# Kernel optimization log

Hardware: AMD Instinct MI355X
Metric: run time of the kernel (lower is better)

## Reference

```python
import jax, jax.numpy as jnp
import numpy as np

KERNEL_MUL = 2.0
KERNEL_NUM = 5


def _cross_entropy(logits, labels):
    logp = jax.nn.log_softmax(logits, axis=-1)
    return -jnp.take_along_axis(logp, labels[:, None], axis=-1).mean()


def _distill_loss(teacher_logits, student_logits):
    t = jax.nn.softmax(teacher_logits, axis=-1)
    return jnp.sum(-t * jax.nn.log_softmax(student_logits, axis=-1), axis=-1).mean()


def _mk_mmd(source, target):
    # Multi-kernel Gaussian MMD (standard DAN-style implementation).
    ns = source.shape[0]
    total = jnp.concatenate([source, target], axis=0)  # [ns+nt, D]
    sq = jnp.sum(total * total, axis=1)
    l2 = sq[:, None] + sq[None, :] - 2.0 * (total @ total.T)  # [n, n]
    n = total.shape[0]
    bandwidth = jnp.sum(l2) / (n * n - n)
    bandwidth = bandwidth / (KERNEL_MUL ** (KERNEL_NUM // 2))
    kernels = jnp.zeros_like(l2)
    for i in range(KERNEL_NUM):
        kernels = kernels + jnp.exp(-l2 / (bandwidth * (KERNEL_MUL ** i)))
    xx = kernels[:ns, :ns]
    yy = kernels[ns:, ns:]
    xy = kernels[:ns, ns:]
    yx = kernels[ns:, :ns]
    return jnp.mean(xx + yy - xy - yx)


def setup_inputs() -> dict:
    key = jax.random.key(0)
    k1, k2, k3, k4, k5 = jax.random.split(key, 5)
    Ns, Nt, D, C = 4096, 4096, 256, 6
    return {
        "source_feature": jax.random.normal(k1, (Ns, D), dtype=jnp.float32),
        "target_feature": jax.random.normal(k2, (Nt, D), dtype=jnp.float32),
        "source_clf": jax.random.normal(k3, (Ns, C), dtype=jnp.float32),
        "target_clf": jax.random.normal(k4, (Nt, C), dtype=jnp.float32),
        "source_label": jax.random.randint(k5, (Ns,), 0, C, dtype=jnp.int64),
    }


def reference(source_feature, target_feature, source_clf, target_clf, source_label):
    clf_loss = _cross_entropy(source_clf, source_label)

    # Pairwise euclidean distance [Ns, Nt] (cdist, p=2)
    ss = jnp.sum(source_feature * source_feature, axis=1)
    tt = jnp.sum(target_feature * target_feature, axis=1)
    d2 = ss[:, None] + tt[None, :] - 2.0 * (source_feature @ target_feature.T)
    dist = jnp.sqrt(jnp.maximum(d2, 0.0))

    min_idx = jnp.argmin(dist, axis=1)    # nearest target for each source
    min_idx_t = jnp.argmin(dist, axis=0)  # nearest source for each target

    dis_loss = _distill_loss(source_clf, target_clf[min_idx, :])
    dis_loss = dis_loss + _distill_loss(source_clf[min_idx_t, :], target_clf)

    transfer_loss = _mk_mmd(source_feature, target_feature)
    return jnp.stack([clf_loss, dis_loss, transfer_loss])
```

## Files before the change

kernel.cpp:

```cpp
#include <hip/hip_runtime.h>
#include <hip/hip_bf16.h>


#define NS 4096
#define D  256
#define C  6

typedef unsigned int u32;
typedef unsigned short u16;
typedef __attribute__((ext_vector_type(8))) short short8;
typedef __attribute__((ext_vector_type(8))) unsigned short ushort8v;
typedef __attribute__((ext_vector_type(4))) float floatx4;
typedef __attribute__((ext_vector_type(2))) float float2v;

#define EXP2F(x) __builtin_amdgcn_exp2f(x)

#define GLD_LDS16(g, l)                                                        \
    __builtin_amdgcn_global_load_lds(                                          \
        (const __attribute__((address_space(1))) unsigned int*)(g),            \
        (__attribute__((address_space(3))) unsigned int*)(l), 16, 0, 0)

__device__ inline u16 f2bf(float f) {
    unsigned u = __float_as_uint(f);
    return (u16)((u + 0x7FFFu + ((u >> 16) & 1u)) >> 16);
}

__global__ __launch_bounds__(256) void kA(const float* __restrict__ src,
                                          const float* __restrict__ tgt,
                                          u16* __restrict__ sb, u16* __restrict__ tb,
                                          float* __restrict__ sq,
                                          u32* __restrict__ rowkey,
                                          u32* __restrict__ colkey,
                                          double* __restrict__ accD,
                                          int* __restrict__ cnts,
                                          float* __restrict__ ssqPart) {
    __shared__ float wsA[4];
    int b = blockIdx.x, t = threadIdx.x;
    int w = t >> 6, l = t & 63;
    int r2 = b * 4 + w;
    int r = r2 * 2 + (l >> 5);
    int lc = (l & 31) * 8;
    const float* row = (r < NS) ? src + (size_t)r * D : tgt + (size_t)(r - NS) * D;
    u16* orow        = (r < NS) ? sb + (size_t)r * D : tb + (size_t)(r - NS) * D;
    float4 v0 = *(const float4*)&row[lc];
    float4 v1 = *(const float4*)&row[lc + 4];
    ushort8v o;
    o.s0 = f2bf(v0.x); o.s1 = f2bf(v0.y); o.s2 = f2bf(v0.z); o.s3 = f2bf(v0.w);
    o.s4 = f2bf(v1.x); o.s5 = f2bf(v1.y); o.s6 = f2bf(v1.z); o.s7 = f2bf(v1.w);
    *(ushort8v*)&orow[lc] = o;
    float s = v0.x * v0.x + v0.y * v0.y + v0.z * v0.z + v0.w * v0.w +
              v1.x * v1.x + v1.y * v1.y + v1.z * v1.z + v1.w * v1.w;
    #pragma unroll
    for (int off = 16; off; off >>= 1) s += __shfl_down(s, off, 64);
    if ((l & 31) == 0) sq[r] = s;

    float rtot = s + __shfl_down(s, 32, 64);
    if (l == 0) wsA[w] = rtot;

    int gid = b * 256 + t;
    if (gid < NS) rowkey[gid] = 0xFFFFFFFFu;
    else if (gid < 2 * NS) colkey[gid - NS] = 0xFFFFFFFFu;
    if (b == 0) {
        if (t < 8) accD[t] = 0.0;
        else if (t == 8) cnts[0] = 0;
    }
    __syncthreads();
    if (t == 0) ssqPart[b] = wsA[0] + wsA[1] + wsA[2] + wsA[3];
}

__global__ __launch_bounds__(256, 3) void k3_mfma(const u16* __restrict__ Sb,
                                                  const u16* __restrict__ Tb,
                                                  const float* __restrict__ sq,
                                                  double* __restrict__ accD,
                                                  u32* __restrict__ rowkey,
                                                  u32* __restrict__ colkey,
                                                  const float* __restrict__ ssqPart) {
    int idx = blockIdx.x;
    int bz, ti, tj;
    if (idx < 1024) {
        bz = 0; ti = idx >> 5; tj = idx & 31;
    } else {
        int t = idx - 1024;
        bz = 1;
        if (t >= 528) { t -= 528; bz = 2; }
        int i = (int)((65.0f - sqrtf(4225.0f - 8.0f * (float)t)) * 0.5f);
        if ((i + 1) * (64 - i) / 2 <= t) i++;
        else if (i * (65 - i) / 2 > t) i--;
        ti = i;
        tj = i + (t - i * (65 - i) / 2);
    }

    const u16* Am = (bz == 2) ? Tb : Sb;
    const u16* Bm = (bz == 1) ? Sb : Tb;
    const float* sqA = (bz == 2) ? sq + NS : sq;
    const float* sqB = (bz == 1) ? sq : sq + NS;
    int zacc = (bz == 0) ? 2 : (bz - 1);

    __shared__ __align__(16) u16 Atile[128 * 64];
    __shared__ __align__(16) u16 Btile[128 * 64];
    __shared__ float sqa_s[128], sqb_s[128];
    __shared__ u32 rminL[128], cminL[128];
    __shared__ float wsum[4];
    __shared__ float wssq[4];

    int tid = threadIdx.x;
    int w = tid >> 6, ln = tid & 63;
    int wm = w >> 1, wn = w & 1;
    int quad = ln >> 4, lrow = ln & 15;
    int row0 = ti * 128, col0 = tj * 128;

    if (tid < 128) { sqa_s[tid] = sqA[row0 + tid]; rminL[tid] = 0xFFFFFFFFu; }
    else           { sqb_s[tid - 128] = sqB[col0 + tid - 128]; cminL[tid - 128] = 0xFFFFFFFFu; }

    float4 pv = *(const float4*)&ssqPart[tid * 4];
    float ssq_p = pv.x + pv.y + pv.z + pv.w;
    #pragma unroll
    for (int off = 32; off; off >>= 1) ssq_p += __shfl_down(ssq_p, off, 64);
    if (ln == 0) wssq[w] = ssq_p;

    int lr8 = ln >> 3;
    int cg  = (ln & 7) ^ lr8;

    floatx4 acc[4][4] = {};

    #pragma unroll 2
    for (int kc = 0; kc < D; kc += 64) {
        #pragma unroll
        for (int i = 0; i < 4; i++) {
            int lrb = w * 32 + i * 8;
            GLD_LDS16(Am + (size_t)(row0 + lrb + lr8) * D + kc + cg * 8,
                      &Atile[lrb * 64]);
            GLD_LDS16(Bm + (size_t)(col0 + lrb + lr8) * D + kc + cg * 8,
                      &Btile[lrb * 64]);
        }
        __syncthreads();
        #pragma unroll
        for (int ks = 0; ks < 2; ks++) {
            int ch = (ks * 4 + quad) ^ (lrow & 7);
            short8 bf4[4];
            #pragma unroll
            for (int cf = 0; cf < 4; cf++)
                bf4[cf] = *(const short8*)&Btile[(wn * 64 + cf * 16 + lrow) * 64 + ch * 8];
            #pragma unroll
            for (int rf = 0; rf < 4; rf++) {
                short8 af = *(const short8*)&Atile[(wm * 64 + rf * 16 + lrow) * 64 + ch * 8];
                #pragma unroll
                for (int cf = 0; cf < 4; cf++)
                    acc[rf][cf] = __builtin_amdgcn_mfma_f32_16x16x32_bf16(
                        af, bf4[cf], acc[rf][cf], 0, 0, 0);
            }
        }
        __syncthreads();
    }

    float ssq = wssq[0] + wssq[1] + wssq[2] + wssq[3];
    float bw = (float)(2.0 * 8192.0 * (double)ssq / (8192.0 * 8192.0 - 8192.0) / 4.0);
    float nlog = -1.4426950408889634f / (bw * 16.0f);
    float m2n  = -2.0f * nlog;
    float2v m2n2 = {m2n, m2n};
    float2v tsum2 = {0.f, 0.f};
    float tsum = 0.f;

    float sbn_c[4];
    #pragma unroll
    for (int cf = 0; cf < 4; cf++)
        sbn_c[cf] = sqb_s[wn * 64 + cf * 16 + lrow] * nlog;

    int rbase = row0 + wm * 64, cbase = col0 + wn * 64;

    if (bz == 0) {
        u32 ck[4];
        #pragma unroll
        for (int cf = 0; cf < 4; cf++) ck[cf] = 0xFFFFFFFFu;
        #pragma unroll
        for (int rf = 0; rf < 4; rf++) {
            int sA = wm * 64 + rf * 16 + quad * 4;
            int giB = rbase + rf * 16 + quad * 4;
            float2v san01 = {sqa_s[sA + 0] * nlog, sqa_s[sA + 1] * nlog};
            float2v san23 = {sqa_s[sA + 2] * nlog, sqa_s[sA + 3] * nlog};
            u32 rk[4];
            #pragma unroll
            for (int reg = 0; reg < 4; reg++) rk[reg] = 0xFFFFFFFFu;
            #pragma unroll
            for (int cf = 0; cf < 4; cf++) {
                int gj = cbase + cf * 16 + lrow;
                float2v sbv2 = {sbn_c[cf], sbn_c[cf]};
                float2v g01 = acc[rf][cf].xy * m2n2 + (san01 + sbv2);
                float2v g23 = acc[rf][cf].zw * m2n2 + (san23 + sbv2);
                float2v t4a, t4b;
                t4a.x = EXP2F(g01.x); t4a.y = EXP2F(g01.y);
                t4b.x = EXP2F(g23.x); t4b.y = EXP2F(g23.y);
                float2v t3a = t4a * t4a, t2a = t3a * t3a, t1a = t2a * t2a, t0a = t1a * t1a;
                float2v t3b = t4b * t4b, t2b = t3b * t3b, t1b = t2b * t2b, t0b = t1b * t1b;
                tsum2 += ((t0a + t1a) + (t2a + t3a)) + t4a;
                tsum2 += ((t0b + t1b) + (t2b + t3b)) + t4b;
                u32 q0 = __float_as_uint(g01.x) & 0xFFFFF000u;
                u32 q1 = __float_as_uint(g01.y) & 0xFFFFF000u;
                u32 q2 = __float_as_uint(g23.x) & 0xFFFFF000u;
                u32 q3 = __float_as_uint(g23.y) & 0xFFFFF000u;
                rk[0] = min(rk[0], q0 | (u32)gj);
                rk[1] = min(rk[1], q1 | (u32)gj);
                rk[2] = min(rk[2], q2 | (u32)gj);
                rk[3] = min(rk[3], q3 | (u32)gj);
                ck[cf] = min(ck[cf], q0 | (u32)(giB + 0));
                ck[cf] = min(ck[cf], q1 | (u32)(giB + 1));
                ck[cf] = min(ck[cf], q2 | (u32)(giB + 2));
                ck[cf] = min(ck[cf], q3 | (u32)(giB + 3));
            }
            #pragma unroll
            for (int reg = 0; reg < 4; reg++) {
                u32 v = rk[reg];
                #pragma unroll
                for (int m = 1; m <= 8; m <<= 1)
                    v = min(v, (u32)__shfl_xor((int)v, m, 64));
                if (lrow == 0)
                    atomicMin(&rminL[wm * 64 + rf * 16 + quad * 4 + reg], v);
            }
        }
        #pragma unroll
        for (int cf = 0; cf < 4; cf++) {
            u32 v = ck[cf];
            v = min(v, (u32)__shfl_xor((int)v, 16, 64));
            v = min(v, (u32)__shfl_xor((int)v, 32, 64));
            if (quad == 0)
                atomicMin(&cminL[wn * 64 + cf * 16 + lrow], v);
        }
    } else if (ti < tj) {
        #pragma unroll
        for (int rf = 0; rf < 4; rf++) {
            int sA = wm * 64 + rf * 16 + quad * 4;
            float2v san01 = {sqa_s[sA + 0] * nlog, sqa_s[sA + 1] * nlog};
            float2v san23 = {sqa_s[sA + 2] * nlog, sqa_s[sA + 3] * nlog};
            #pragma unroll
            for (int cf = 0; cf < 4; cf++) {
                float2v sbv2 = {sbn_c[cf], sbn_c[cf]};
                float2v g01 = acc[rf][cf].xy * m2n2 + (san01 + sbv2);
                float2v g23 = acc[rf][cf].zw * m2n2 + (san23 + sbv2);
                float2v t4a, t4b;
                t4a.x = EXP2F(g01.x); t4a.y = EXP2F(g01.y);
                t4b.x = EXP2F(g23.x); t4b.y = EXP2F(g23.y);
                float2v t3a = t4a * t4a, t2a = t3a * t3a, t1a = t2a * t2a, t0a = t1a * t1a;
                float2v t3b = t4b * t4b, t2b = t3b * t3b, t1b = t2b * t2b, t0b = t1b * t1b;
                tsum2 += ((t0a + t1a) + (t2a + t3a)) + t4a;
                tsum2 += ((t0b + t1b) + (t2b + t3b)) + t4b;
            }
        }
    } else {
        #pragma unroll
        for (int rf = 0; rf < 4; rf++) {
            float san[4];
            #pragma unroll
            for (int reg = 0; reg < 4; reg++)
                san[reg] = sqa_s[wm * 64 + rf * 16 + quad * 4 + reg] * nlog;
            #pragma unroll
            for (int cf = 0; cf < 4; cf++) {
                int gj = cbase + cf * 16 + lrow;
                float sbv = sbn_c[cf];
                #pragma unroll
                for (int reg = 0; reg < 4; reg++) {
                    int gi = rbase + rf * 16 + quad * 4 + reg;
                    float arg = fmaf(acc[rf][cf][reg], m2n, san[reg] + sbv);
                    float t4 = EXP2F(arg);
                    float t3 = t4 * t4, t2 = t3 * t3, t1 = t2 * t2, t0 = t1 * t1;
                    if (gi < gj)
                        tsum += t0 + t1 + t2 + t3 + t4;
                }
            }
        }
    }

    tsum += tsum2.x + tsum2.y;
    #pragma unroll
    for (int off = 32; off; off >>= 1) tsum += __shfl_down(tsum, off, 64);
    if (ln == 0) wsum[w] = tsum;
    __syncthreads();
    if (tid == 0)
        atomicAdd(&accD[zacc], (double)(wsum[0] + wsum[1] + wsum[2] + wsum[3]));
    if (bz == 0) {
        if (tid < 128) atomicMin(&rowkey[row0 + tid], rminL[tid]);
        else           atomicMin(&colkey[col0 + tid - 128], cminL[tid - 128]);
    }
}

__global__ __launch_bounds__(256) void k4(const float* __restrict__ sclf,
                                          const float* __restrict__ tclf,
                                          const int* __restrict__ label,
                                          const u32* __restrict__ rowkey,
                                          const u32* __restrict__ colkey,
                                          double* __restrict__ accD,
                                          int* __restrict__ cnts,
                                          float* __restrict__ out) {
    if (blockIdx.x == 16) {
        if (threadIdx.x == 0) {
            while (atomicAdd(&cnts[0], 0) < 16) __builtin_amdgcn_s_sleep(2);
            double Sxx  = atomicAdd(&accD[0], 0.0);
            double Syy  = atomicAdd(&accD[1], 0.0);
            double Sxy  = atomicAdd(&accD[2], 0.0);
            double clfS = atomicAdd(&accD[3], 0.0);
            double disS = atomicAdd(&accD[4], 0.0);
            double ns = (double)NS;
            out[0] = (float)(clfS / ns);
            out[1] = (float)(disS / ns);
            double sum_xx = 2.0 * Sxx + ns * 5.0;
            double sum_yy = 2.0 * Syy + ns * 5.0;
            out[2] = (float)((sum_xx + sum_yy - 2.0 * Sxy) / (ns * ns));
        }
        return;
    }

    int i = blockIdx.x * 256 + threadIdx.x;
    float clf, dis = 0.f;

    const float* x = sclf + (size_t)i * C;
    float mx = x[0];
    #pragma unroll
    for (int c = 1; c < C; c++) mx = fmaxf(mx, x[c]);
    float sx = 0.f;
    #pragma unroll
    for (int c = 0; c < C; c++) sx += __expf(x[c] - mx);
    clf = mx + __logf(sx) - x[label[i]];

    {
        int j = (int)(rowkey[i] & 0xFFFu);
        const float* y = tclf + (size_t)j * C;
        float my = y[0];
        #pragma unroll
        for (int c = 1; c < C; c++) my = fmaxf(my, y[c]);
        float sy = 0.f;
        #pragma unroll
        for (int c = 0; c < C; c++) sy += __expf(y[c] - my);
        float dot = 0.f;
        #pragma unroll
        for (int c = 0; c < C; c++) dot += __expf(x[c] - mx) * y[c];
        dis += my + __logf(sy) - dot / sx;
    }
    {
        int it = (int)(colkey[i] & 0xFFFu);
        const float* xt = sclf + (size_t)it * C;
        float mt = xt[0];
        #pragma unroll
        for (int c = 1; c < C; c++) mt = fmaxf(mt, xt[c]);
        float st = 0.f;
        #pragma unroll
        for (int c = 0; c < C; c++) st += __expf(xt[c] - mt);
        const float* zz = tclf + (size_t)i * C;
        float mz = zz[0];
        #pragma unroll
        for (int c = 1; c < C; c++) mz = fmaxf(mz, zz[c]);
        float sz = 0.f;
        #pragma unroll
        for (int c = 0; c < C; c++) sz += __expf(zz[c] - mz);
        float dot2 = 0.f;
        #pragma unroll
        for (int c = 0; c < C; c++) dot2 += __expf(xt[c] - mt) * zz[c];
        dis += mz + __logf(sz) - dot2 / st;
    }

    #pragma unroll
    for (int off = 32; off; off >>= 1) {
        clf += __shfl_down(clf, off, 64);
        dis += __shfl_down(dis, off, 64);
    }
    if ((threadIdx.x & 63) == 0) {
        atomicAdd(&accD[3], (double)clf);
        atomicAdd(&accD[4], (double)dis);
    }
    __syncthreads();
    if (threadIdx.x == 0) atomicAdd(&cnts[0], 1);
}

extern "C" void kernel_launch(void* const* d_in, const int* in_sizes, int n_in,
                              void* d_out, int out_size, void* d_ws, size_t ws_size,
                              hipStream_t stream) {
    const float* src  = (const float*)d_in[0];
    const float* tgt  = (const float*)d_in[1];
    const float* sclf = (const float*)d_in[2];
    const float* tclf = (const float*)d_in[3];
    const int*   lab  = (const int*)d_in[4];
    float* out = (float*)d_out;

    char* ws = (char*)d_ws;
    u16* sb     = (u16*)ws;
    u16* tb     = sb + (size_t)NS * D;
    u32* rowkey = (u32*)(ws + 2 * (size_t)NS * D * 2);
    u32* colkey = rowkey + NS;
    float* sq   = (float*)(colkey + NS);
    double* accD = (double*)((char*)sq + 2 * NS * 4 + 64);
    int* cnts    = (int*)(accD + 8);
    float* ssqPart = (float*)(accD + 16);

    kA<<<1024, 256, 0, stream>>>(src, tgt, sb, tb, sq, rowkey, colkey, accD, cnts, ssqPart);
    k3_mfma<<<2080, 256, 0, stream>>>(sb, tb, sq, accD, rowkey, colkey, ssqPart);
    k4<<<17, 256, 0, stream>>>(sclf, tclf, lab, rowkey, colkey, accD, cnts, out);
}
```

Baseline: 113.5 us.

## Fuse final loss kernel into MFMA kernel using completion counters

Removes the separate k4 launch by appending 17 extra blocks to the MFMA kernel grid. Sixteen of them spin on a counter until all 1024 cross-distance tiles have published their argmin keys, then compute the classification and distillation losses. The last block waits for all tiles and loss blocks before writing the outputs. This saves one launch and lets the loss work overlap with the MMD tiles, but it relies on in-kernel spin-waits, which could deadlock or waste CU slots if the waiting blocks get scheduled before the tiles they wait on.

```diff
diff --git a/kernel.cpp b/kernel.cpp
--- a/kernel.cpp
+++ b/kernel.cpp
@@ -62,7 +62,7 @@
     else if (gid < 2 * NS) colkey[gid - NS] = 0xFFFFFFFFu;
     if (b == 0) {
         if (t < 8) accD[t] = 0.0;
-        else if (t == 8) cnts[0] = 0;
+        else if (t >= 8 && t < 12) cnts[t - 8] = 0;
     }
     __syncthreads();
     if (t == 0) ssqPart[b] = wsA[0] + wsA[1] + wsA[2] + wsA[3];
@@ -74,8 +74,104 @@
                                                   double* __restrict__ accD,
                                                   u32* __restrict__ rowkey,
                                                   u32* __restrict__ colkey,
-                                                  const float* __restrict__ ssqPart) {
+                                                  const float* __restrict__ ssqPart,
+                                                  const float* __restrict__ sclf,
+                                                  const float* __restrict__ tclf,
+                                                  const int* __restrict__ label,
+                                                  int* __restrict__ cnts,
+                                                  float* __restrict__ out) {
     int idx = blockIdx.x;
+    int tid = threadIdx.x;
+
+    if (idx >= 2080) {
+        int widx = idx - 2080;
+        if (widx < 16) {
+            if (tid == 0)
+                while (atomicAdd(&cnts[0], 0) < 1024) __builtin_amdgcn_s_sleep(8);
+            __syncthreads();
+
+            int i = widx * 256 + tid;
+            float clf, dis = 0.f;
+
+            const float* x = sclf + (size_t)i * C;
+            float mx = x[0];
+            #pragma unroll
+            for (int c = 1; c < C; c++) mx = fmaxf(mx, x[c]);
+            float sx = 0.f;
+            #pragma unroll
+            for (int c = 0; c < C; c++) sx += __expf(x[c] - mx);
+            clf = mx + __logf(sx) - x[label[i]];
+
+            u32 rkv = atomicAdd(&rowkey[i], 0u);
+            u32 ckv = atomicAdd(&colkey[i], 0u);
+
+            {
+                int j = (int)(rkv & 0xFFFu);
+                const float* y = tclf + (size_t)j * C;
+                float my = y[0];
+                #pragma unroll
+                for (int c = 1; c < C; c++) my = fmaxf(my, y[c]);
+                float sy = 0.f;
+                #pragma unroll
+                for (int c = 0; c < C; c++) sy += __expf(y[c] - my);
+                float dot = 0.f;
+                #pragma unroll
+                for (int c = 0; c < C; c++) dot += __expf(x[c] - mx) * y[c];
+                dis += my + __logf(sy) - dot / sx;
+            }
+            {
+                int it = (int)(ckv & 0xFFFu);
+                const float* xt = sclf + (size_t)it * C;
+                float mt = xt[0];
+                #pragma unroll
+                for (int c = 1; c < C; c++) mt = fmaxf(mt, xt[c]);
+                float st = 0.f;
+                #pragma unroll
+                for (int c = 0; c < C; c++) st += __expf(xt[c] - mt);
+                const float* zz = tclf + (size_t)i * C;
+                float mz = zz[0];
+                #pragma unroll
+                for (int c = 1; c < C; c++) mz = fmaxf(mz, zz[c]);
+                float sz = 0.f;
+                #pragma unroll
+                for (int c = 0; c < C; c++) sz += __expf(zz[c] - mz);
+                float dot2 = 0.f;
+                #pragma unroll
+                for (int c = 0; c < C; c++) dot2 += __expf(xt[c] - mt) * zz[c];
+                dis += mz + __logf(sz) - dot2 / st;
+            }
+
+            #pragma unroll
+            for (int off = 32; off; off >>= 1) {
+                clf += __shfl_down(clf, off, 64);
+                dis += __shfl_down(dis, off, 64);
+            }
+            if ((tid & 63) == 0) {
+                atomicAdd(&accD[3], (double)clf);
+                atomicAdd(&accD[4], (double)dis);
+            }
+            __syncthreads();
+            if (tid == 0) atomicAdd(&cnts[2], 1);
+        } else {
+            if (tid == 0) {
+                while (atomicAdd(&cnts[1], 0) < 2080 ||
+                       atomicAdd(&cnts[2], 0) < 16) __builtin_amdgcn_s_sleep(8);
+                double Sxx  = atomicAdd(&accD[0], 0.0);
+                double Syy  = atomicAdd(&accD[1], 0.0);
+                double Sxy  = atomicAdd(&accD[2], 0.0);
+                double clfS = atomicAdd(&accD[3], 0.0);
+                double disS = atomicAdd(&accD[4], 0.0);
+                double ns = (double)NS;
+                out[0] = (float)(clfS / ns);
+                out[1] = (float)(disS / ns);
+                double sum_xx = 2.0 * Sxx + ns * 5.0;
+                double sum_yy = 2.0 * Syy + ns * 5.0;
+                out[2] = (float)((sum_xx + sum_yy - 2.0 * Sxy) / (ns * ns));
+            }
+        }
+        return;
+    }
+
     int bz, ti, tj;
     if (idx < 1024) {
         bz = 0; ti = idx >> 5; tj = idx & 31;
@@ -103,7 +199,6 @@
     __shared__ float wsum[4];
     __shared__ float wssq[4];
 
-    int tid = threadIdx.x;
     int w = tid >> 6, ln = tid & 63;
     int wm = w >> 1, wn = w & 1;
     int quad = ln >> 4, lrow = ln & 15;
@@ -280,93 +375,12 @@
         if (tid < 128) atomicMin(&rowkey[row0 + tid], rminL[tid]);
         else           atomicMin(&colkey[col0 + tid - 128], cminL[tid - 128]);
     }
-}
-
-__global__ __launch_bounds__(256) void k4(const float* __restrict__ sclf,
-                                          const float* __restrict__ tclf,
-                                          const int* __restrict__ label,
-                                          const u32* __restrict__ rowkey,
-                                          const u32* __restrict__ colkey,
-                                          double* __restrict__ accD,
-                                          int* __restrict__ cnts,
-                                          float* __restrict__ out) {
-    if (blockIdx.x == 16) {
-        if (threadIdx.x == 0) {
-            while (atomicAdd(&cnts[0], 0) < 16) __builtin_amdgcn_s_sleep(2);
-            double Sxx  = atomicAdd(&accD[0], 0.0);
-            double Syy  = atomicAdd(&accD[1], 0.0);
-            double Sxy  = atomicAdd(&accD[2], 0.0);
-            double clfS = atomicAdd(&accD[3], 0.0);
-            double disS = atomicAdd(&accD[4], 0.0);
-            double ns = (double)NS;
-            out[0] = (float)(clfS / ns);
-            out[1] = (float)(disS / ns);
-            double sum_xx = 2.0 * Sxx + ns * 5.0;
-            double sum_yy = 2.0 * Syy + ns * 5.0;
-            out[2] = (float)((sum_xx + sum_yy - 2.0 * Sxy) / (ns * ns));
-        }
-        return;
-    }
-
-    int i = blockIdx.x * 256 + threadIdx.x;
-    float clf, dis = 0.f;
-
-    const float* x = sclf + (size_t)i * C;
-    float mx = x[0];
-    #pragma unroll
-    for (int c = 1; c < C; c++) mx = fmaxf(mx, x[c]);
-    float sx = 0.f;
-    #pragma unroll
-    for (int c = 0; c < C; c++) sx += __expf(x[c] - mx);
-    clf = mx + __logf(sx) - x[label[i]];
-
-    {
-        int j = (int)(rowkey[i] & 0xFFFu);
-        const float* y = tclf + (size_t)j * C;
-        float my = y[0];
-        #pragma unroll
-        for (int c = 1; c < C; c++) my = fmaxf(my, y[c]);
-        float sy = 0.f;
-        #pragma unroll
-        for (int c = 0; c < C; c++) sy += __expf(y[c] - my);
-        float dot = 0.f;
-        #pragma unroll
-        for (int c = 0; c < C; c++) dot += __expf(x[c] - mx) * y[c];
-        dis += my + __logf(sy) - dot / sx;
-    }
-    {
-        int it = (int)(colkey[i] & 0xFFFu);
-        const float* xt = sclf + (size_t)it * C;
-        float mt = xt[0];
-        #pragma unroll
-        for (int c = 1; c < C; c++) mt = fmaxf(mt, xt[c]);
-        float st = 0.f;
-        #pragma unroll
-        for (int c = 0; c < C; c++) st += __expf(xt[c] - mt);
-        const float* zz = tclf + (size_t)i * C;
-        float mz = zz[0];
-        #pragma unroll
-        for (int c = 1; c < C; c++) mz = fmaxf(mz, zz[c]);
-        float sz = 0.f;
-        #pragma unroll
-        for (int c = 0; c < C; c++) sz += __expf(zz[c] - mz);
-        float dot2 = 0.f;
-        #pragma unroll
-        for (int c = 0; c < C; c++) dot2 += __expf(xt[c] - mt) * zz[c];
-        dis += mz + __logf(sz) - dot2 / st;
-    }
-
-    #pragma unroll
-    for (int off = 32; off; off >>= 1) {
-        clf += __shfl_down(clf, off, 64);
-        dis += __shfl_down(dis, off, 64);
-    }
-    if ((threadIdx.x & 63) == 0) {
-        atomicAdd(&accD[3], (double)clf);
-        atomicAdd(&accD[4], (double)dis);
-    }
+
     __syncthreads();
-    if (threadIdx.x == 0) atomicAdd(&cnts[0], 1);
+    if (tid == 0) {
+        if (bz == 0) atomicAdd(&cnts[0], 1);
+        atomicAdd(&cnts[1], 1);
+    }
 }
 
 extern "C" void kernel_launch(void* const* d_in, const int* in_sizes, int n_in,
@@ -390,6 +404,6 @@
     float* ssqPart = (float*)(accD + 16);
 
     kA<<<1024, 256, 0, stream>>>(src, tgt, sb, tb, sq, rowkey, colkey, accD, cnts, ssqPart);
-    k3_mfma<<<2080, 256, 0, stream>>>(sb, tb, sq, accD, rowkey, colkey, ssqPart);
-    k4<<<17, 256, 0, stream>>>(sclf, tclf, lab, rowkey, colkey, accD, cnts, out);
+    k3_mfma<<<2097, 256, 0, stream>>>(sb, tb, sq, accD, rowkey, colkey, ssqPart,
+                                      sclf, tclf, lab, cnts, out);
 }
```

Result: slower. 136.5 us (+20.3%).

## Double-buffer LDS tiles with 32-wide K chunks to overlap loads with MFMA

Applied to the files above, without the earlier changes.

Replaces the single-buffered 64-wide K loop, which had two barriers per step, with a double-buffered 32-wide K pipeline. The next chunk's global-to-LDS loads are issued before computing on the current buffer, and only one barrier remains per step. The LDS swizzle changes to a 4-chunk XOR pattern to suit the narrower rows. The aim is to hide global load latency behind MFMA work, at the cost of more loop iterations and barriers in total, with the same LDS footprint.

```diff
diff --git a/kernel.cpp b/kernel.cpp
--- a/kernel.cpp
+++ b/kernel.cpp
@@ -96,8 +96,8 @@
     const float* sqB = (bz == 1) ? sq : sq + NS;
     int zacc = (bz == 0) ? 2 : (bz - 1);
 
-    __shared__ __align__(16) u16 Atile[128 * 64];
-    __shared__ __align__(16) u16 Btile[128 * 64];
+    __shared__ __align__(16) u16 At[2][128 * 32];
+    __shared__ __align__(16) u16 Bt[2][128 * 32];
     __shared__ float sqa_s[128], sqb_s[128];
     __shared__ u32 rminL[128], cminL[128];
     __shared__ float wsum[4];
@@ -118,39 +118,47 @@
     for (int off = 32; off; off >>= 1) ssq_p += __shfl_down(ssq_p, off, 64);
     if (ln == 0) wssq[w] = ssq_p;
 
-    int lr8 = ln >> 3;
-    int cg  = (ln & 7) ^ lr8;
+    int srow = ln >> 2;
+    int cgn  = (ln & 3) ^ ((ln >> 3) & 3);
+    int chq  = quad ^ ((lrow >> 1) & 3);
 
     floatx4 acc[4][4] = {};
 
-    #pragma unroll 2
-    for (int kc = 0; kc < D; kc += 64) {
-        #pragma unroll
-        for (int i = 0; i < 4; i++) {
-            int lrb = w * 32 + i * 8;
-            GLD_LDS16(Am + (size_t)(row0 + lrb + lr8) * D + kc + cg * 8,
-                      &Atile[lrb * 64]);
-            GLD_LDS16(Bm + (size_t)(col0 + lrb + lr8) * D + kc + cg * 8,
-                      &Btile[lrb * 64]);
-        }
-        __syncthreads();
-        #pragma unroll
-        for (int ks = 0; ks < 2; ks++) {
-            int ch = (ks * 4 + quad) ^ (lrow & 7);
-            short8 bf4[4];
+    #pragma unroll
+    for (int i = 0; i < 2; i++) {
+        int lrb = i * 64 + w * 16;
+        GLD_LDS16(Am + (size_t)(row0 + lrb + srow) * D + 0 + cgn * 8, &At[0][lrb * 32]);
+        GLD_LDS16(Bm + (size_t)(col0 + lrb + srow) * D + 0 + cgn * 8, &Bt[0][lrb * 32]);
+    }
+    __syncthreads();
+
+    #pragma unroll
+    for (int p = 0; p < 8; p++) {
+        const int cur = p & 1, nxt = cur ^ 1;
+        if (p < 7) {
+            int kc = (p + 1) * 32;
+            #pragma unroll
+            for (int i = 0; i < 2; i++) {
+                int lrb = i * 64 + w * 16;
+                GLD_LDS16(Am + (size_t)(row0 + lrb + srow) * D + kc + cgn * 8,
+                          &At[nxt][lrb * 32]);
+                GLD_LDS16(Bm + (size_t)(col0 + lrb + srow) * D + kc + cgn * 8,
+                          &Bt[nxt][lrb * 32]);
+            }
+        }
+        short8 bf4[4];
+        #pragma unroll
+        for (int cf = 0; cf < 4; cf++)
+            bf4[cf] = *(const short8*)&Bt[cur][(wn * 64 + cf * 16 + lrow) * 32 + chq * 8];
+        #pragma unroll
+        for (int rf = 0; rf < 4; rf++) {
+            short8 af = *(const short8*)&At[cur][(wm * 64 + rf * 16 + lrow) * 32 + chq * 8];
             #pragma unroll
             for (int cf = 0; cf < 4; cf++)
-                bf4[cf] = *(const short8*)&Btile[(wn * 64 + cf * 16 + lrow) * 64 + ch * 8];
-            #pragma unroll
-            for (int rf = 0; rf < 4; rf++) {
-                short8 af = *(const short8*)&Atile[(wm * 64 + rf * 16 + lrow) * 64 + ch * 8];
-                #pragma unroll
-                for (int cf = 0; cf < 4; cf++)
-                    acc[rf][cf] = __builtin_amdgcn_mfma_f32_16x16x32_bf16(
-                        af, bf4[cf], acc[rf][cf], 0, 0, 0);
-            }
-        }
-        __syncthreads();
+                acc[rf][cf] = __builtin_amdgcn_mfma_f32_16x16x32_bf16(
+                    af, bf4[cf], acc[rf][cf], 0, 0, 0);
+        }
+        if (p < 7) __syncthreads();
     }
 
     float ssq = wssq[0] + wssq[1] + wssq[2] + wssq[3];
```

Measured after the change: 116.7 us. 2.8% more time.
